# Kernel tuning notes

Hardware: AMD Instinct MI355X
Metric: run time of the kernel (lower is better)

The kernel has to match this reference:

```python
import jax, jax.numpy as jnp
import numpy as np

B, T, C, H, W = 1, 8, 128, 64, 64
F = 64  # num_feat


def setup_inputs() -> dict:
    key = jax.random.key(0)
    ks = jax.random.split(key, 8)
    return {
        "input1": jax.random.normal(ks[0], (B, T, C, H, W), jnp.float32),
        "input2": jax.random.normal(ks[1], (B, T, C, H, W), jnp.float32),
        "W1": jax.random.normal(ks[2], (F, C), jnp.float32) * 0.05,
        "b1": jax.random.normal(ks[3], (F,), jnp.float32) * 0.05,
        "W2": jax.random.normal(ks[4], (F, C), jnp.float32) * 0.05,
        "b2": jax.random.normal(ks[5], (F,), jnp.float32) * 0.05,
        "W3": jax.random.normal(ks[6], (F, C), jnp.float32) * 0.05,
        "b3": jax.random.normal(ks[7], (F,), jnp.float32) * 0.05,
    }


def reference(input1, input2, W1, b1, W2, b2, W3, b3):
    # act == 0 (ReLU branch). Conv1d(kernel=1) == per-position linear projection.
    b, t, c, h, w = input1.shape
    n = h * w
    x1 = input1.reshape(b, t, c, n)  # matches transpose(1,2).reshape then frame slice
    x2 = input2.reshape(b, t, c, n)
    q = jnp.einsum('fc,btcn->btnf', W1, x1) + b1          # [B,T,N,F]
    k = jnp.einsum('fc,btcn->btnf', W2, x2) + b2          # [B,T,N,F]
    g = jnp.einsum('fc,btcn->btnf', W3, x1) + b3          # [B,T,N,F]
    scores = jax.nn.relu(jnp.einsum('btnf,btmf->btnm', q, k))  # [B,T,N,N]
    out = jnp.einsum('btnm,btmf->btnf', scores, g)        # [B,T,N,F]
    # view([B,H,W,F]).permute(0,3,1,2), stacked over T -> [B,T,F,H,W]
    return out.reshape(b, t, h, w, -1).transpose(0, 1, 4, 2, 3)
```

## Files before the change

kernel.cpp:

```cpp
#include <hip/hip_runtime.h>
#include <hip/hip_bf16.h>

constexpr int T = 8;
constexpr int C = 128;
constexpr int N = 4096;
constexpr int F = 64;

typedef __bf16 bf16x8 __attribute__((ext_vector_type(8)));
typedef __bf16 bf16x4 __attribute__((ext_vector_type(4)));
typedef float  f32x4  __attribute__((ext_vector_type(4)));

__global__ __launch_bounds__(256) void prep_w_kernel(
    const float* __restrict__ W1, const float* __restrict__ W2,
    const float* __restrict__ W3, __bf16* __restrict__ Wb)
{
    int i = blockIdx.x * 256 + threadIdx.x;
    const float* Ws[3] = {W1, W2, W3};
    int p = i >> 13, r = i & 8191;
    Wb[i] = (__bf16)Ws[p][r];
}

__global__ __launch_bounds__(256) void zero_out_kernel(float* __restrict__ out)
{
    int i = blockIdx.x * 256 + threadIdx.x;
    ((f32x4*)out)[i] = (f32x4){0.f, 0.f, 0.f, 0.f};
}

__global__ __launch_bounds__(256) void proj_kernel(
    const float* __restrict__ x1, const float* __restrict__ x2,
    const __bf16* __restrict__ Wb,
    const float* __restrict__ b1, const float* __restrict__ b2,
    const float* __restrict__ b3,
    __bf16* __restrict__ Qb, __bf16* __restrict__ Kb, __bf16* __restrict__ Gw)
{
    const int t  = blockIdx.x >> 6;
    const int nb = blockIdx.x & 63;
    const int n0 = nb * 64;

    constexpr int XS = C + 8;
    __shared__ __bf16 Xt1[64 * XS];
    __shared__ __bf16 Xt2[64 * XS];

    const int tid = threadIdx.x;
#pragma unroll
    for (int rep = 0; rep < 32; ++rep) {
        int idx = rep * 256 + tid;
        int c = idx >> 6, nl = idx & 63;
        size_t goff = ((size_t)t * C + c) * (size_t)N + n0 + nl;
        Xt1[nl * XS + c] = (__bf16)x1[goff];
        Xt2[nl * XS + c] = (__bf16)x2[goff];
    }
    __syncthreads();

    const int wave = tid >> 6, lane = tid & 63;
    const int quad = lane >> 4, l16 = lane & 15;

    bf16x8 a1[4], a2[4];
#pragma unroll
    for (int cc = 0; cc < 4; ++cc) {
        a1[cc] = *(const bf16x8*)&Xt1[(wave * 16 + l16) * XS + cc * 32 + quad * 8];
        a2[cc] = *(const bf16x8*)&Xt2[(wave * 16 + l16) * XS + cc * 32 + quad * 8];
    }

#pragma unroll
    for (int p = 0; p < 2; ++p) {
        const __bf16* W    = Wb + (size_t)p * F * C;
        const float*  bias = p ? b2 : b1;
        __bf16*       O    = p ? Kb : Qb;

        f32x4 acc[4];
#pragma unroll
        for (int ft = 0; ft < 4; ++ft) acc[ft] = (f32x4){0.f, 0.f, 0.f, 0.f};
#pragma unroll
        for (int cc = 0; cc < 4; ++cc) {
#pragma unroll
            for (int ft = 0; ft < 4; ++ft) {
                bf16x8 b = *(const bf16x8*)&W[(ft * 16 + l16) * C + cc * 32 + quad * 8];
                bf16x8 a = p ? a2[cc] : a1[cc];
                acc[ft] = __builtin_amdgcn_mfma_f32_16x16x32_bf16(a, b, acc[ft], 0, 0, 0);
            }
        }
#pragma unroll
        for (int ft = 0; ft < 4; ++ft) {
            int f = ft * 16 + l16;
            float bv = bias[f];
#pragma unroll
            for (int r = 0; r < 4; ++r) {
                int n = n0 + wave * 16 + quad * 4 + r;
                O[((size_t)t * N + n) * F + f] = (__bf16)(acc[ft][r] + bv);
            }
        }
    }

    {
        const __bf16* W3b = Wb + (size_t)2 * F * C;
        bf16x8 wa[4];
#pragma unroll
        for (int cc = 0; cc < 4; ++cc)
            wa[cc] = *(const bf16x8*)&W3b[(wave * 16 + l16) * C + cc * 32 + quad * 8];

        f32x4 acc[4];
#pragma unroll
        for (int nt = 0; nt < 4; ++nt) acc[nt] = (f32x4){0.f, 0.f, 0.f, 0.f};
#pragma unroll
        for (int cc = 0; cc < 4; ++cc) {
#pragma unroll
            for (int nt = 0; nt < 4; ++nt) {
                bf16x8 b = *(const bf16x8*)&Xt1[(nt * 16 + l16) * XS + cc * 32 + quad * 8];
                acc[nt] = __builtin_amdgcn_mfma_f32_16x16x32_bf16(wa[cc], b, acc[nt], 0, 0, 0);
            }
        }
#pragma unroll
        for (int nt = 0; nt < 4; ++nt) {
#pragma unroll
            for (int r = 0; r < 4; ++r) {
                int f = wave * 16 + quad * 4 + r;
                int n = n0 + nt * 16 + l16;
                Gw[((size_t)t * F + f) * (size_t)N + n] = (__bf16)(acc[nt][r] + b3[f]);
            }
        }
    }
}

constexpr int KSPLIT = 2;

__global__ __launch_bounds__(256) void attn_kernel(
    const __bf16* __restrict__ Qb, const __bf16* __restrict__ Kb,
    const __bf16* __restrict__ Gw, float* __restrict__ out)
{
    const int ks = blockIdx.x & (KSPLIT - 1);
    const int qb = (blockIdx.x / KSPLIT) & 31;
    const int t  = blockIdx.x / (KSPLIT * 32);
    const int q0 = qb * 128;

    constexpr int KS = 72;
    __shared__ __bf16 Kt[64 * KS];
    __shared__ __bf16 Gt[64 * KS];
    __shared__ __bf16 Sb[128 * KS];

    const int tid = threadIdx.x, wave = tid >> 6, lane = tid & 63;
    const int quad = lane >> 4, l16 = lane & 15;

    bf16x8 qf[2][2];
#pragma unroll
    for (int qg = 0; qg < 2; ++qg) {
        const __bf16* qrow = &Qb[((size_t)t * N + q0 + wave * 32 + qg * 16 + l16) * F];
        qf[qg][0] = *(const bf16x8*)&qrow[quad * 8];
        qf[qg][1] = *(const bf16x8*)&qrow[32 + quad * 8];
    }

    f32x4 oacc[4][2];
#pragma unroll
    for (int ft = 0; ft < 4; ++ft)
#pragma unroll
        for (int qg = 0; qg < 2; ++qg) oacc[ft][qg] = (f32x4){0.f, 0.f, 0.f, 0.f};

    const int kb_lo = ks * (N / 64 / KSPLIT);
    const int kb_hi = kb_lo + (N / 64 / KSPLIT);

    const int r8a = tid >> 3,          c8a = (tid & 7) * 8;
    const int r8b = (tid + 256) >> 3,  c8b = c8a;

    bf16x8 kv0, kv1, gv0, gv1;
    {
        const int k0 = kb_lo * 64;
        kv0 = *(const bf16x8*)&Kb[((size_t)t * N + k0 + r8a) * F + c8a];
        kv1 = *(const bf16x8*)&Kb[((size_t)t * N + k0 + r8b) * F + c8b];
        gv0 = *(const bf16x8*)&Gw[((size_t)t * F + r8a) * (size_t)N + k0 + c8a];
        gv1 = *(const bf16x8*)&Gw[((size_t)t * F + r8b) * (size_t)N + k0 + c8b];
    }

    for (int kb = kb_lo; kb < kb_hi; ++kb) {
        __syncthreads();
        *(bf16x8*)&Kt[r8a * KS + c8a] = kv0;
        *(bf16x8*)&Kt[r8b * KS + c8b] = kv1;
        *(bf16x8*)&Gt[r8a * KS + c8a] = gv0;
        *(bf16x8*)&Gt[r8b * KS + c8b] = gv1;
        __syncthreads();

        if (kb + 1 < kb_hi) {
            const int k0 = (kb + 1) * 64;
            kv0 = *(const bf16x8*)&Kb[((size_t)t * N + k0 + r8a) * F + c8a];
            kv1 = *(const bf16x8*)&Kb[((size_t)t * N + k0 + r8b) * F + c8b];
            gv0 = *(const bf16x8*)&Gw[((size_t)t * F + r8a) * (size_t)N + k0 + c8a];
            gv1 = *(const bf16x8*)&Gw[((size_t)t * F + r8b) * (size_t)N + k0 + c8b];
        }

#pragma unroll
        for (int nt = 0; nt < 4; ++nt) {
            bf16x8 k0f = *(const bf16x8*)&Kt[(nt * 16 + l16) * KS + quad * 8];
            bf16x8 k1f = *(const bf16x8*)&Kt[(nt * 16 + l16) * KS + 32 + quad * 8];
#pragma unroll
            for (int qg = 0; qg < 2; ++qg) {
                f32x4 s = (f32x4){0.f, 0.f, 0.f, 0.f};
                s = __builtin_amdgcn_mfma_f32_16x16x32_bf16(k0f, qf[qg][0], s, 0, 0, 0);
                s = __builtin_amdgcn_mfma_f32_16x16x32_bf16(k1f, qf[qg][1], s, 0, 0, 0);
                bf16x4 sp;
#pragma unroll
                for (int r = 0; r < 4; ++r) sp[r] = (__bf16)fmaxf(s[r], 0.f);
                *(bf16x4*)&Sb[(wave * 32 + qg * 16 + l16) * KS + nt * 16 + quad * 4] = sp;
            }
        }

        bf16x8 sf[2][2];
#pragma unroll
        for (int qg = 0; qg < 2; ++qg) {
            const __bf16* srow = &Sb[(wave * 32 + qg * 16 + l16) * KS];
            sf[qg][0] = *(const bf16x8*)&srow[quad * 8];
            sf[qg][1] = *(const bf16x8*)&srow[32 + quad * 8];
        }
#pragma unroll
        for (int ft = 0; ft < 4; ++ft) {
            bf16x8 g0 = *(const bf16x8*)&Gt[(ft * 16 + l16) * KS + quad * 8];
            bf16x8 g1 = *(const bf16x8*)&Gt[(ft * 16 + l16) * KS + 32 + quad * 8];
#pragma unroll
            for (int qg = 0; qg < 2; ++qg) {
                oacc[ft][qg] = __builtin_amdgcn_mfma_f32_16x16x32_bf16(g0, sf[qg][0], oacc[ft][qg], 0, 0, 0);
                oacc[ft][qg] = __builtin_amdgcn_mfma_f32_16x16x32_bf16(g1, sf[qg][1], oacc[ft][qg], 0, 0, 0);
            }
        }
    }

#pragma unroll
    for (int ft = 0; ft < 4; ++ft)
#pragma unroll
        for (int qg = 0; qg < 2; ++qg)
#pragma unroll
            for (int r = 0; r < 4; ++r) {
                int f = ft * 16 + quad * 4 + r;
                int q = q0 + wave * 32 + qg * 16 + l16;
                unsafeAtomicAdd(&out[((size_t)t * F + f) * (size_t)N + q], oacc[ft][qg][r]);
            }
}

extern "C" void kernel_launch(void* const* d_in, const int* in_sizes, int n_in,
                              void* d_out, int out_size, void* d_ws, size_t ws_size,
                              hipStream_t stream) {
    const float* x1 = (const float*)d_in[0];
    const float* x2 = (const float*)d_in[1];
    const float* W1 = (const float*)d_in[2];
    const float* b1 = (const float*)d_in[3];
    const float* W2 = (const float*)d_in[4];
    const float* b2 = (const float*)d_in[5];
    const float* W3 = (const float*)d_in[6];
    const float* b3 = (const float*)d_in[7];
    float* out = (float*)d_out;

    __bf16* Qb = (__bf16*)d_ws;
    __bf16* Kb = Qb + (size_t)T * N * F;
    __bf16* Gw = Kb + (size_t)T * N * F;
    __bf16* Wb = Gw + (size_t)T * N * F;

    prep_w_kernel<<<dim3(3 * F * C / 256), dim3(256), 0, stream>>>(W1, W2, W3, Wb);
    proj_kernel<<<dim3(T * (N / 64)), dim3(256), 0, stream>>>(
        x1, x2, Wb, b1, b2, b3, Qb, Kb, Gw);
    zero_out_kernel<<<dim3(T * F * N / 4 / 256), dim3(256), 0, stream>>>(out);
    attn_kernel<<<dim3(T * 32 * KSPLIT), dim3(256), 0, stream>>>(Qb, Kb, Gw, out);
}
```

Measured before the change: 163.5 us.

## Rewrite attention kernel with 32x32 MFMA, register-resident scores and in-block K-split reduction

The attention kernel now uses 512-thread blocks where 8 waves split the key range four ways. K and G fragments are loaded straight from global memory into registers with double buffering, replacing the shared-memory staging and per-tile barriers. ReLU scores stay in registers and are repacked with v_permlane32_swap into the B operand of 32x32x16 MFMAs, so the score round-trip through LDS disappears. Partial outputs are reduced in shared memory and written once with vector stores, which removes the zero-fill kernel and the global atomics. This trades more register pressure and redundant global and L2 traffic for K/G loads against fewer barriers and launches.

```diff
diff --git a/kernel.cpp b/kernel.cpp
--- a/kernel.cpp
+++ b/kernel.cpp
@@ -8,7 +8,9 @@
 
 typedef __bf16 bf16x8 __attribute__((ext_vector_type(8)));
 typedef __bf16 bf16x4 __attribute__((ext_vector_type(4)));
+typedef __bf16 bf16x2 __attribute__((ext_vector_type(2)));
 typedef float  f32x4  __attribute__((ext_vector_type(4)));
+typedef float  f32x16 __attribute__((ext_vector_type(16)));
 
 __global__ __launch_bounds__(256) void prep_w_kernel(
     const float* __restrict__ W1, const float* __restrict__ W2,
@@ -18,12 +20,6 @@
     const float* Ws[3] = {W1, W2, W3};
     int p = i >> 13, r = i & 8191;
     Wb[i] = (__bf16)Ws[p][r];
-}
-
-__global__ __launch_bounds__(256) void zero_out_kernel(float* __restrict__ out)
-{
-    int i = blockIdx.x * 256 + threadIdx.x;
-    ((f32x4*)out)[i] = (f32x4){0.f, 0.f, 0.f, 0.f};
 }
 
 __global__ __launch_bounds__(256) void proj_kernel(
@@ -122,115 +118,157 @@
     }
 }
 
-constexpr int KSPLIT = 2;
-
-__global__ __launch_bounds__(256) void attn_kernel(
+
+#define PACK_PS(SACC, PS0, PS1)                                              \
+    {                                                                        \
+        unsigned P[8];                                                       \
+        _Pragma("unroll")                                                    \
+        for (int m = 0; m < 8; ++m) {                                        \
+            union { bf16x2 h; unsigned u; } pk_;                             \
+            pk_.h[0] = (__bf16)fmaxf(SACC[2 * m], 0.f);                      \
+            pk_.h[1] = (__bf16)fmaxf(SACC[2 * m + 1], 0.f);                  \
+            P[m] = pk_.u;                                                    \
+        }                                                                    \
+        asm("v_permlane32_swap_b32 %0, %1" : "+v"(P[0]), "+v"(P[2]));        \
+        asm("v_permlane32_swap_b32 %0, %1" : "+v"(P[1]), "+v"(P[3]));        \
+        asm("v_permlane32_swap_b32 %0, %1" : "+v"(P[4]), "+v"(P[6]));        \
+        asm("v_permlane32_swap_b32 %0, %1" : "+v"(P[5]), "+v"(P[7]));        \
+        union { unsigned u[4]; bf16x8 v; } lo_, hi_;                         \
+        lo_.u[0] = P[0]; lo_.u[1] = P[1]; lo_.u[2] = P[2]; lo_.u[3] = P[3];  \
+        hi_.u[0] = P[4]; hi_.u[1] = P[5]; hi_.u[2] = P[6]; hi_.u[3] = P[7];  \
+        PS0 = lo_.v; PS1 = hi_.v;                                            \
+    }
+
+#define ATTN_STEP(KF, KN)                                                    \
+    {                                                                        \
+        _Pragma("unroll")                                                    \
+        for (int c = 0; c < 4; ++c)                                          \
+            _Pragma("unroll")                                                \
+            for (int ft = 0; ft < 2; ++ft)                                   \
+                gf[c][ft] = *(const bf16x8*)(gptr + (size_t)ft * 32 * N + kb + c * 16); \
+        bf16x8 ps[4];                                                        \
+        _Pragma("unroll")                                                    \
+        for (int kt = 0; kt < 2; ++kt) {                                     \
+            f32x16 s;                                                        \
+            _Pragma("unroll")                                                \
+            for (int r = 0; r < 16; ++r) s[r] = 0.f;                         \
+            _Pragma("unroll")                                                \
+            for (int fc = 0; fc < 4; ++fc)                                   \
+                s = __builtin_amdgcn_mfma_f32_32x32x16_bf16(KF[kt][fc], qf[0][fc], s, 0, 0, 0); \
+            PACK_PS(s, ps[kt * 2], ps[kt * 2 + 1])                           \
+        }                                                                    \
+        _Pragma("unroll")                                                    \
+        for (int kt = 0; kt < 2; ++kt)                                       \
+            _Pragma("unroll")                                                \
+            for (int fc = 0; fc < 4; ++fc)                                   \
+                KN[kt][fc] = *(const bf16x8*)(kptr + (size_t)(kbn + kt * 32) * F + fc * 16); \
+        _Pragma("unroll")                                                    \
+        for (int c = 0; c < 4; ++c)                                          \
+            _Pragma("unroll")                                                \
+            for (int ft = 0; ft < 2; ++ft)                                   \
+                oacc[0][ft] = __builtin_amdgcn_mfma_f32_32x32x16_bf16(gf[c][ft], ps[c], oacc[0][ft], 0, 0, 0); \
+        _Pragma("unroll")                                                    \
+        for (int kt = 0; kt < 2; ++kt) {                                     \
+            f32x16 s;                                                        \
+            _Pragma("unroll")                                                \
+            for (int r = 0; r < 16; ++r) s[r] = 0.f;                         \
+            _Pragma("unroll")                                                \
+            for (int fc = 0; fc < 4; ++fc)                                   \
+                s = __builtin_amdgcn_mfma_f32_32x32x16_bf16(KF[kt][fc], qf[1][fc], s, 0, 0, 0); \
+            PACK_PS(s, ps[kt * 2], ps[kt * 2 + 1])                           \
+        }                                                                    \
+        _Pragma("unroll")                                                    \
+        for (int c = 0; c < 4; ++c)                                          \
+            _Pragma("unroll")                                                \
+            for (int ft = 0; ft < 2; ++ft)                                   \
+                oacc[1][ft] = __builtin_amdgcn_mfma_f32_32x32x16_bf16(gf[c][ft], ps[c], oacc[1][ft], 0, 0, 0); \
+        kb  = kbn;                                                           \
+        kbn = (kbn + 64 < kw0 + N / 4) ? kbn + 64 : kw0;                     \
+    }
+
+__global__ __launch_bounds__(512, 2) void attn_kernel(
     const __bf16* __restrict__ Qb, const __bf16* __restrict__ Kb,
     const __bf16* __restrict__ Gw, float* __restrict__ out)
 {
-    const int ks = blockIdx.x & (KSPLIT - 1);
-    const int qb = (blockIdx.x / KSPLIT) & 31;
-    const int t  = blockIdx.x / (KSPLIT * 32);
+    const int t  = blockIdx.x & 7;
+    const int qb = blockIdx.x >> 3;
     const int q0 = qb * 128;
 
-    constexpr int KS = 72;
-    __shared__ __bf16 Kt[64 * KS];
-    __shared__ __bf16 Gt[64 * KS];
-    __shared__ __bf16 Sb[128 * KS];
-
-    const int tid = threadIdx.x, wave = tid >> 6, lane = tid & 63;
-    const int quad = lane >> 4, l16 = lane & 15;
-
-    bf16x8 qf[2][2];
-#pragma unroll
-    for (int qg = 0; qg < 2; ++qg) {
-        const __bf16* qrow = &Qb[((size_t)t * N + q0 + wave * 32 + qg * 16 + l16) * F];
-        qf[qg][0] = *(const bf16x8*)&qrow[quad * 8];
-        qf[qg][1] = *(const bf16x8*)&qrow[32 + quad * 8];
-    }
-
-    f32x4 oacc[4][2];
-#pragma unroll
-    for (int ft = 0; ft < 4; ++ft)
-#pragma unroll
-        for (int qg = 0; qg < 2; ++qg) oacc[ft][qg] = (f32x4){0.f, 0.f, 0.f, 0.f};
-
-    const int kb_lo = ks * (N / 64 / KSPLIT);
-    const int kb_hi = kb_lo + (N / 64 / KSPLIT);
-
-    const int r8a = tid >> 3,          c8a = (tid & 7) * 8;
-    const int r8b = (tid + 256) >> 3,  c8b = c8a;
-
-    bf16x8 kv0, kv1, gv0, gv1;
-    {
-        const int k0 = kb_lo * 64;
-        kv0 = *(const bf16x8*)&Kb[((size_t)t * N + k0 + r8a) * F + c8a];
-        kv1 = *(const bf16x8*)&Kb[((size_t)t * N + k0 + r8b) * F + c8b];
-        gv0 = *(const bf16x8*)&Gw[((size_t)t * F + r8a) * (size_t)N + k0 + c8a];
-        gv1 = *(const bf16x8*)&Gw[((size_t)t * F + r8b) * (size_t)N + k0 + c8b];
-    }
-
-    for (int kb = kb_lo; kb < kb_hi; ++kb) {
-        __syncthreads();
-        *(bf16x8*)&Kt[r8a * KS + c8a] = kv0;
-        *(bf16x8*)&Kt[r8b * KS + c8b] = kv1;
-        *(bf16x8*)&Gt[r8a * KS + c8a] = gv0;
-        *(bf16x8*)&Gt[r8b * KS + c8b] = gv1;
-        __syncthreads();
-
-        if (kb + 1 < kb_hi) {
-            const int k0 = (kb + 1) * 64;
-            kv0 = *(const bf16x8*)&Kb[((size_t)t * N + k0 + r8a) * F + c8a];
-            kv1 = *(const bf16x8*)&Kb[((size_t)t * N + k0 + r8b) * F + c8b];
-            gv0 = *(const bf16x8*)&Gw[((size_t)t * F + r8a) * (size_t)N + k0 + c8a];
-            gv1 = *(const bf16x8*)&Gw[((size_t)t * F + r8b) * (size_t)N + k0 + c8b];
-        }
-
-#pragma unroll
-        for (int nt = 0; nt < 4; ++nt) {
-            bf16x8 k0f = *(const bf16x8*)&Kt[(nt * 16 + l16) * KS + quad * 8];
-            bf16x8 k1f = *(const bf16x8*)&Kt[(nt * 16 + l16) * KS + 32 + quad * 8];
-#pragma unroll
-            for (int qg = 0; qg < 2; ++qg) {
-                f32x4 s = (f32x4){0.f, 0.f, 0.f, 0.f};
-                s = __builtin_amdgcn_mfma_f32_16x16x32_bf16(k0f, qf[qg][0], s, 0, 0, 0);
-                s = __builtin_amdgcn_mfma_f32_16x16x32_bf16(k1f, qf[qg][1], s, 0, 0, 0);
-                bf16x4 sp;
-#pragma unroll
-                for (int r = 0; r < 4; ++r) sp[r] = (__bf16)fmaxf(s[r], 0.f);
-                *(bf16x4*)&Sb[(wave * 32 + qg * 16 + l16) * KS + nt * 16 + quad * 4] = sp;
-            }
-        }
-
-        bf16x8 sf[2][2];
-#pragma unroll
-        for (int qg = 0; qg < 2; ++qg) {
-            const __bf16* srow = &Sb[(wave * 32 + qg * 16 + l16) * KS];
-            sf[qg][0] = *(const bf16x8*)&srow[quad * 8];
-            sf[qg][1] = *(const bf16x8*)&srow[32 + quad * 8];
-        }
-#pragma unroll
-        for (int ft = 0; ft < 4; ++ft) {
-            bf16x8 g0 = *(const bf16x8*)&Gt[(ft * 16 + l16) * KS + quad * 8];
-            bf16x8 g1 = *(const bf16x8*)&Gt[(ft * 16 + l16) * KS + 32 + quad * 8];
-#pragma unroll
-            for (int qg = 0; qg < 2; ++qg) {
-                oacc[ft][qg] = __builtin_amdgcn_mfma_f32_16x16x32_bf16(g0, sf[qg][0], oacc[ft][qg], 0, 0, 0);
-                oacc[ft][qg] = __builtin_amdgcn_mfma_f32_16x16x32_bf16(g1, sf[qg][1], oacc[ft][qg], 0, 0, 0);
-            }
-        }
-    }
-
-#pragma unroll
-    for (int ft = 0; ft < 4; ++ft)
+    const int tid  = threadIdx.x;
+    const int wave = tid >> 6, lane = tid & 63;
+    const int m32  = lane & 31, hi = lane >> 5;
+    const int qh   = wave & 1;
+    const int ksl  = wave >> 1;
+    const int kw0  = ksl * (N / 4);
+
+    __shared__ __align__(16) float red[2][64][68];
+
+    bf16x8 qf[2][4];
+    {
+        const __bf16* qptr = Qb + ((size_t)t * N + q0 + qh * 64 + m32) * F + hi * 8;
 #pragma unroll
         for (int qg = 0; qg < 2; ++qg)
 #pragma unroll
-            for (int r = 0; r < 4; ++r) {
-                int f = ft * 16 + quad * 4 + r;
-                int q = q0 + wave * 32 + qg * 16 + l16;
-                unsafeAtomicAdd(&out[((size_t)t * F + f) * (size_t)N + q], oacc[ft][qg][r]);
-            }
+            for (int fc = 0; fc < 4; ++fc)
+                qf[qg][fc] = *(const bf16x8*)(qptr + qg * 32 * F + fc * 16);
+    }
+
+    f32x16 oacc[2][2];
+#pragma unroll
+    for (int qg = 0; qg < 2; ++qg)
+#pragma unroll
+        for (int ft = 0; ft < 2; ++ft)
+#pragma unroll
+            for (int r = 0; r < 16; ++r) oacc[qg][ft][r] = 0.f;
+
+    const __bf16* kptr = Kb + ((size_t)t * N + m32) * F + hi * 8;
+    const __bf16* gptr = Gw + ((size_t)t * F + m32) * (size_t)N + hi * 8;
+
+    bf16x8 kfA[2][4], kfB[2][4], gf[4][2];
+
+#pragma unroll
+    for (int kt = 0; kt < 2; ++kt)
+#pragma unroll
+        for (int fc = 0; fc < 4; ++fc)
+            kfA[kt][fc] = *(const bf16x8*)(kptr + (size_t)(kw0 + kt * 32) * F + fc * 16);
+
+    int kb = kw0, kbn = kw0 + 64;
+
+#pragma unroll 1
+    for (int it = 0; it < 8; ++it) {
+        ATTN_STEP(kfA, kfB)
+        ATTN_STEP(kfB, kfA)
+    }
+
+#pragma unroll
+    for (int i = 0; i < 17; ++i)
+        ((float*)red)[i * 512 + tid] = 0.f;
+    __syncthreads();
+
+    {
+        float* buf = &red[qh][0][0];
+#pragma unroll
+        for (int qg = 0; qg < 2; ++qg)
+#pragma unroll
+            for (int ft = 0; ft < 2; ++ft)
+#pragma unroll
+                for (int r = 0; r < 16; ++r) {
+                    int f = ft * 32 + (r & 3) + 8 * (r >> 2) + 4 * hi;
+                    atomicAdd(&buf[f * 68 + qg * 32 + m32], oacc[qg][ft][r]);
+                }
+    }
+    __syncthreads();
+
+    {
+        const int qh_t = tid >> 8;
+        const int fr   = (tid >> 2) & 63;
+        const int qq   = tid & 3;
+        const float* rp = &red[qh_t][fr][qq * 16];
+        float* op = out + ((size_t)t * F + fr) * (size_t)N + q0 + qh_t * 64 + qq * 16;
+#pragma unroll
+        for (int j = 0; j < 4; ++j)
+            *(f32x4*)(op + 4 * j) = *(const f32x4*)(rp + 4 * j);
+    }
 }
 
 extern "C" void kernel_launch(void* const* d_in, const int* in_sizes, int n_in,
@@ -254,6 +292,5 @@
     prep_w_kernel<<<dim3(3 * F * C / 256), dim3(256), 0, stream>>>(W1, W2, W3, Wb);
     proj_kernel<<<dim3(T * (N / 64)), dim3(256), 0, stream>>>(
         x1, x2, Wb, b1, b2, b3, Qb, Kb, Gw);
-    zero_out_kernel<<<dim3(T * F * N / 4 / 256), dim3(256), 0, stream>>>(out);
-    attn_kernel<<<dim3(T * 32 * KSPLIT), dim3(256), 0, stream>>>(Qb, Kb, Gw, out);
-}
+    attn_kernel<<<dim3(T * (N / 128)), dim3(512), 0, stream>>>(Qb, Kb, Gw, out);
+}
```

Result: slower. 216.2 us (+32.2%).

## Vectorize projection loads and stores, reuse X fragments for G, raise KSPLIT

Applied to the files above, without the earlier changes.

The projection kernel now loads x1/x2 as float4 and writes transposed bf16x4 into shared memory. MFMA operands are swapped so each lane holds contiguous output features, which lets Q/K/G be written as 4-wide bf16 vectors instead of scalar stores. The G projection reuses the already-loaded X register fragments instead of rereading shared memory. Attention split-K goes from 2 to 4 for more parallelism, at the cost of more atomic or partial-sum traffic on the output.

```diff
diff --git a/kernel.cpp b/kernel.cpp
--- a/kernel.cpp
+++ b/kernel.cpp
@@ -15,9 +15,9 @@
     const float* __restrict__ W3, __bf16* __restrict__ Wb)
 {
     int i = blockIdx.x * 256 + threadIdx.x;
-    const float* Ws[3] = {W1, W2, W3};
     int p = i >> 13, r = i & 8191;
-    Wb[i] = (__bf16)Ws[p][r];
+    const float* W = (p == 0) ? W1 : (p == 1) ? W2 : W3;
+    Wb[i] = (__bf16)W[r];
 }
 
 __global__ __launch_bounds__(256) void zero_out_kernel(float* __restrict__ out)
@@ -37,18 +37,35 @@
     const int nb = blockIdx.x & 63;
     const int n0 = nb * 64;
 
-    constexpr int XS = C + 8;
+    constexpr int XS = 136;
     __shared__ __bf16 Xt1[64 * XS];
     __shared__ __bf16 Xt2[64 * XS];
 
     const int tid = threadIdx.x;
-#pragma unroll
-    for (int rep = 0; rep < 32; ++rep) {
-        int idx = rep * 256 + tid;
-        int c = idx >> 6, nl = idx & 63;
-        size_t goff = ((size_t)t * C + c) * (size_t)N + n0 + nl;
-        Xt1[nl * XS + c] = (__bf16)x1[goff];
-        Xt2[nl * XS + c] = (__bf16)x2[goff];
+    const int ng  = tid & 15;
+    const int cgi = tid >> 4;
+
+#pragma unroll
+    for (int pass = 0; pass < 2; ++pass) {
+        const int c0 = cgi * 4 + pass * 64;
+        const size_t base = ((size_t)t * C + c0) * (size_t)N + n0 + ng * 4;
+        f32x4 v1[4], v2[4];
+#pragma unroll
+        for (int i = 0; i < 4; ++i) {
+            v1[i] = *(const f32x4*)&x1[base + (size_t)i * N];
+            v2[i] = *(const f32x4*)&x2[base + (size_t)i * N];
+        }
+#pragma unroll
+        for (int j = 0; j < 4; ++j) {
+            bf16x4 o1, o2;
+#pragma unroll
+            for (int i = 0; i < 4; ++i) {
+                o1[i] = (__bf16)v1[i][j];
+                o2[i] = (__bf16)v2[i][j];
+            }
+            *(bf16x4*)&Xt1[(ng * 4 + j) * XS + c0] = o1;
+            *(bf16x4*)&Xt2[(ng * 4 + j) * XS + c0] = o2;
+        }
     }
     __syncthreads();
 
@@ -75,54 +92,50 @@
         for (int cc = 0; cc < 4; ++cc) {
 #pragma unroll
             for (int ft = 0; ft < 4; ++ft) {
-                bf16x8 b = *(const bf16x8*)&W[(ft * 16 + l16) * C + cc * 32 + quad * 8];
-                bf16x8 a = p ? a2[cc] : a1[cc];
-                acc[ft] = __builtin_amdgcn_mfma_f32_16x16x32_bf16(a, b, acc[ft], 0, 0, 0);
-            }
-        }
+                bf16x8 wf = *(const bf16x8*)&W[(ft * 16 + l16) * C + cc * 32 + quad * 8];
+                bf16x8 xf = p ? a2[cc] : a1[cc];
+                acc[ft] = __builtin_amdgcn_mfma_f32_16x16x32_bf16(wf, xf, acc[ft], 0, 0, 0);
+            }
+        }
+        const int n = n0 + wave * 16 + l16;
 #pragma unroll
         for (int ft = 0; ft < 4; ++ft) {
-            int f = ft * 16 + l16;
-            float bv = bias[f];
-#pragma unroll
-            for (int r = 0; r < 4; ++r) {
-                int n = n0 + wave * 16 + quad * 4 + r;
-                O[((size_t)t * N + n) * F + f] = (__bf16)(acc[ft][r] + bv);
-            }
+            const int f0 = ft * 16 + quad * 4;
+            f32x4 bv = *(const f32x4*)&bias[f0];
+            bf16x4 o;
+#pragma unroll
+            for (int r = 0; r < 4; ++r) o[r] = (__bf16)(acc[ft][r] + bv[r]);
+            *(bf16x4*)&O[((size_t)t * N + n) * F + f0] = o;
         }
     }
 
     {
         const __bf16* W3b = Wb + (size_t)2 * F * C;
-        bf16x8 wa[4];
-#pragma unroll
-        for (int cc = 0; cc < 4; ++cc)
-            wa[cc] = *(const bf16x8*)&W3b[(wave * 16 + l16) * C + cc * 32 + quad * 8];
-
         f32x4 acc[4];
 #pragma unroll
-        for (int nt = 0; nt < 4; ++nt) acc[nt] = (f32x4){0.f, 0.f, 0.f, 0.f};
+        for (int ft = 0; ft < 4; ++ft) acc[ft] = (f32x4){0.f, 0.f, 0.f, 0.f};
 #pragma unroll
         for (int cc = 0; cc < 4; ++cc) {
 #pragma unroll
-            for (int nt = 0; nt < 4; ++nt) {
-                bf16x8 b = *(const bf16x8*)&Xt1[(nt * 16 + l16) * XS + cc * 32 + quad * 8];
-                acc[nt] = __builtin_amdgcn_mfma_f32_16x16x32_bf16(wa[cc], b, acc[nt], 0, 0, 0);
-            }
-        }
-#pragma unroll
-        for (int nt = 0; nt < 4; ++nt) {
-#pragma unroll
-            for (int r = 0; r < 4; ++r) {
-                int f = wave * 16 + quad * 4 + r;
-                int n = n0 + nt * 16 + l16;
-                Gw[((size_t)t * F + f) * (size_t)N + n] = (__bf16)(acc[nt][r] + b3[f]);
-            }
-        }
-    }
-}
-
-constexpr int KSPLIT = 2;
+            for (int ft = 0; ft < 4; ++ft) {
+                bf16x8 wf = *(const bf16x8*)&W3b[(ft * 16 + l16) * C + cc * 32 + quad * 8];
+                acc[ft] = __builtin_amdgcn_mfma_f32_16x16x32_bf16(a1[cc], wf, acc[ft], 0, 0, 0);
+            }
+        }
+        const int nr0 = n0 + wave * 16 + quad * 4;
+#pragma unroll
+        for (int ft = 0; ft < 4; ++ft) {
+            const int f = ft * 16 + l16;
+            const float bv = b3[f];
+            bf16x4 o;
+#pragma unroll
+            for (int r = 0; r < 4; ++r) o[r] = (__bf16)(acc[ft][r] + bv);
+            *(bf16x4*)&Gw[((size_t)t * F + f) * (size_t)N + nr0] = o;
+        }
+    }
+}
+
+constexpr int KSPLIT = 4;
 
 __global__ __launch_bounds__(256) void attn_kernel(
     const __bf16* __restrict__ Qb, const __bf16* __restrict__ Kb,
```

Result: faster. 156.5 us (-4.3%).
